# Performance work log

Hardware: AMD Instinct MI355X
Metric: run time of the kernel (lower is better)

The kernel has to match this reference:

```python
import jax, jax.numpy as jnp
import numpy as np

B, N_IN, N_OUT, K, V = 8, 2048, 2048, 64, 64


def setup_inputs() -> dict:
    key = jax.random.key(0)
    k1, k2, k3 = jax.random.split(key, 3)
    return {
        "key": jax.random.normal(k1, (B, N_IN, 1, K), dtype=jnp.float32),
        "query": jax.random.normal(k2, (B, 1, N_OUT, K), dtype=jnp.float32),
        "value": jax.random.normal(k3, (B, N_IN, V), dtype=jnp.float32),
    }


def reference(key, query, value):
    ks = key.shape[-1]
    # sum(key * query, 3) / sqrt(key_size)  ==  batched GEMM over key_size
    # weights: [B, n_inputs, n_outputs]
    weights = jnp.einsum("bik,bok->bio", key[:, :, 0, :], query[:, 0, :, :]) / jnp.sqrt(
        jnp.asarray(ks, dtype=key.dtype)
    )
    weights = jax.nn.softmax(weights, axis=1)  # softmax over n_inputs
    # sum(weights[...,None] * value[:,:,None,:], 1) -> [B, n_outputs, value_size]
    vals = jnp.einsum("bio,biv->bov", weights, value)
    # row-wise L2 normalize each [value_size] vector
    vals = vals / (jnp.linalg.norm(vals, axis=-1, keepdims=True) + 1e-12)
    values = jnp.swapaxes(vals, 1, 2)  # [B, value_size, n_outputs]
    return values, weights
```

## Files before the change

### kernel.cpp

```cpp
#include <hip/hip_runtime.h>

#define NB 8
#define NN 2048
#define KK 64
#define VV 64
#define TO 64
#define IT 64
#define NSTEP (NN / IT)
#define SCALE 0.18033688011112043f

typedef __bf16 bfrag __attribute__((ext_vector_type(8)));
typedef float f32x4 __attribute__((ext_vector_type(4)));
typedef unsigned short u16x4 __attribute__((ext_vector_type(4)));
typedef unsigned short u16x8 __attribute__((ext_vector_type(8)));

__device__ __forceinline__ unsigned short bf16r(float f) {
  unsigned u = __float_as_uint(f);
  u += 0x7fffu + ((u >> 16) & 1u);
  return (unsigned short)(u >> 16);
}

__device__ __forceinline__ int swz(int row, int colByte) {
  return row * 128 + (colByte ^ ((row & 7) << 4));
}

__device__ __forceinline__ bfrag lds_frag(const unsigned short* base, int row, int colByte) {
  return *reinterpret_cast<const bfrag*>(reinterpret_cast<const char*>(base) + swz(row, colByte));
}

struct KS { float4 f[4]; };
__device__ __forceinline__ void k_load(KS& s, const float* __restrict__ g) {
  const float4* p = reinterpret_cast<const float4*>(g);
  s.f[0] = p[0]; s.f[1] = p[1]; s.f[2] = p[2]; s.f[3] = p[3];
}
__device__ __forceinline__ void k_write(const KS& s, unsigned short* lds, int row, int colByte) {
  const float* f = reinterpret_cast<const float*>(&s.f[0]);
  u16x8 a, b;
#pragma unroll
  for (int j = 0; j < 8; ++j) a[j] = bf16r(f[j]);
#pragma unroll
  for (int j = 0; j < 8; ++j) b[j] = bf16r(f[8 + j]);
  *reinterpret_cast<u16x8*>(reinterpret_cast<char*>(lds) + swz(row, colByte)) = a;
  *reinterpret_cast<u16x8*>(reinterpret_cast<char*>(lds) + swz(row, colByte + 16)) = b;
}

struct VS { float4 f[4]; };
__device__ __forceinline__ void v_load(VS& s, const float* __restrict__ g) {
  const float4* p = reinterpret_cast<const float4*>(g);
  s.f[0] = p[0]; s.f[1] = p[1];
  const float4* q = reinterpret_cast<const float4*>(g + VV);
  s.f[2] = q[0]; s.f[3] = q[1];
}
__device__ __forceinline__ void v_write(const VS& s, unsigned short* lds, int il, int v0) {
  const float* lo = reinterpret_cast<const float*>(&s.f[0]);
  const float* hi = reinterpret_cast<const float*>(&s.f[2]);
#pragma unroll
  for (int j = 0; j < 8; ++j) {
    unsigned pk = (unsigned)bf16r(lo[j]) | ((unsigned)bf16r(hi[j]) << 16);
    *reinterpret_cast<unsigned*>(reinterpret_cast<char*>(lds) + swz(v0 + j, il * 2)) = pk;
  }
}

__global__ void __launch_bounds__(256) attn_fused(
    const float* __restrict__ key, const float* __restrict__ query,
    const float* __restrict__ value, float* __restrict__ out)
{
  __shared__ __align__(16) unsigned short Kt[2][IT * KK];
  __shared__ __align__(16) unsigned short Vt[2][VV * IT];
  __shared__ __align__(16) unsigned short Qt[TO * KK];
  __shared__ __align__(16) unsigned short Et[TO * IT];
  __shared__ float Red[4][TO];
  __shared__ float BcD[TO];
  __shared__ float BcN[TO];

  const int tid  = threadIdx.x;
  const int lane = tid & 63;
  const int wv   = tid >> 6;
  const int l15  = lane & 15;
  const int l4   = lane >> 4;

  const int b  = blockIdx.x & 7;
  const int o0 = (blockIdx.x >> 3) * TO;

  const float* Kg = key   + (size_t)b * NN * KK;
  const float* Qg = query + (size_t)b * NN * KK;
  const float* Vg = value + (size_t)b * NN * VV;
  float* outV = out + (size_t)b * VV * NN;
  float* outW = out + (size_t)NB * VV * NN + (size_t)b * NN * NN;

  const int krow = tid >> 2;
  const int kel  = (tid & 3) * 16;
  const int kcb  = (tid & 3) * 32;
  const int vil  = (tid & 31) * 2;
  const int vv0  = (tid >> 5) * 8;

  {
    KS qs;
    k_load(qs, Qg + (size_t)(o0 + krow) * KK + kel);
    k_write(qs, Qt, krow, kcb);
  }
  KS ks; VS vs;
  k_load(ks, Kg + (size_t)krow * KK + kel);
  v_load(vs, Vg + (size_t)vil * VV + vv0);
  k_write(ks, Kt[0], krow, kcb);
  v_write(vs, Vt[0], vil, vv0);
  __syncthreads();

  f32x4 uacc[4];
  float Dacc[4] = {0.f, 0.f, 0.f, 0.f};
#pragma unroll
  for (int s = 0; s < 4; ++s) { f32x4 z = {0.f, 0.f, 0.f, 0.f}; uacc[s] = z; }

  for (int t = 0; t < NSTEP; ++t) {
    const int c = t & 1;
    if (t + 1 < NSTEP) {
      k_load(ks, Kg + (size_t)((t + 1) * IT + krow) * KK + kel);
      v_load(vs, Vg + (size_t)((t + 1) * IT + vil) * VV + vv0);
    }
    bfrag a0 = lds_frag(Kt[c], wv * 16 + l15, l4 * 16);
    bfrag a1 = lds_frag(Kt[c], wv * 16 + l15, 64 + l4 * 16);
#pragma unroll
    for (int s = 0; s < 4; ++s) {
      bfrag b0 = lds_frag(Qt, s * 16 + l15, l4 * 16);
      bfrag b1 = lds_frag(Qt, s * 16 + l15, 64 + l4 * 16);
      f32x4 z = {0.f, 0.f, 0.f, 0.f};
      z = __builtin_amdgcn_mfma_f32_16x16x32_bf16(a0, b0, z, 0, 0, 0);
      z = __builtin_amdgcn_mfma_f32_16x16x32_bf16(a1, b1, z, 0, 0, 0);
      f32x4 e;
#pragma unroll
      for (int r = 0; r < 4; ++r) e[r] = exp2f(z[r] * SCALE);
      Dacc[s] += e[0] + e[1] + e[2] + e[3];
      u16x4 pk;
#pragma unroll
      for (int r = 0; r < 4; ++r) pk[r] = bf16r(e[r]);
      *reinterpret_cast<u16x4*>(reinterpret_cast<char*>(Et) +
                                swz(s * 16 + l15, wv * 32 + l4 * 8)) = pk;
    }
    if (t + 1 < NSTEP) {
      k_write(ks, Kt[c ^ 1], krow, kcb);
      v_write(vs, Vt[c ^ 1], vil, vv0);
    }
    __syncthreads();
    bfrag va0 = lds_frag(Vt[c], wv * 16 + l15, l4 * 16);
    bfrag va1 = lds_frag(Vt[c], wv * 16 + l15, 64 + l4 * 16);
#pragma unroll
    for (int s = 0; s < 4; ++s) {
      bfrag e0 = lds_frag(Et, s * 16 + l15, l4 * 16);
      bfrag e1 = lds_frag(Et, s * 16 + l15, 64 + l4 * 16);
      uacc[s] = __builtin_amdgcn_mfma_f32_16x16x32_bf16(va0, e0, uacc[s], 0, 0, 0);
      uacc[s] = __builtin_amdgcn_mfma_f32_16x16x32_bf16(va1, e1, uacc[s], 0, 0, 0);
    }
    __syncthreads();
  }

#pragma unroll
  for (int s = 0; s < 4; ++s) {
    float d = Dacc[s];
    d += __shfl_xor(d, 16, 64);
    d += __shfl_xor(d, 32, 64);
    if (lane < 16) Red[wv][s * 16 + lane] = d;
  }
  __syncthreads();
  if (tid < TO) {
    float D = Red[0][tid] + Red[1][tid] + Red[2][tid] + Red[3][tid];
    BcD[tid] = 1.0f / D;
  }
  __syncthreads();
  float invd[4];
#pragma unroll
  for (int s = 0; s < 4; ++s) invd[s] = BcD[s * 16 + l15];
  __syncthreads();

#pragma unroll
  for (int s = 0; s < 4; ++s) {
    float ss = uacc[s][0] * uacc[s][0] + uacc[s][1] * uacc[s][1] +
               uacc[s][2] * uacc[s][2] + uacc[s][3] * uacc[s][3];
    ss += __shfl_xor(ss, 16, 64);
    ss += __shfl_xor(ss, 32, 64);
    if (lane < 16) Red[wv][s * 16 + lane] = ss;
  }
  __syncthreads();
  if (tid < TO) {
    float n = Red[0][tid] + Red[1][tid] + Red[2][tid] + Red[3][tid];
    BcN[tid] = 1.0f / (sqrtf(n) + 1e-12f);
  }
  __syncthreads();
#pragma unroll
  for (int s = 0; s < 4; ++s) {
    float inn = BcN[s * 16 + l15];
    float* vp = outV + (size_t)(wv * 16 + l4 * 4) * NN + o0 + s * 16 + l15;
#pragma unroll
    for (int r = 0; r < 4; ++r) vp[(size_t)r * NN] = uacc[s][r] * inn;
  }

  k_load(ks, Kg + (size_t)krow * KK + kel);
  k_write(ks, Kt[0], krow, kcb);
  __syncthreads();
  for (int t = 0; t < NSTEP; ++t) {
    const int c = t & 1;
    if (t + 1 < NSTEP)
      k_load(ks, Kg + (size_t)((t + 1) * IT + krow) * KK + kel);
    bfrag a0 = lds_frag(Kt[c], wv * 16 + l15, l4 * 16);
    bfrag a1 = lds_frag(Kt[c], wv * 16 + l15, 64 + l4 * 16);
#pragma unroll
    for (int s = 0; s < 4; ++s) {
      bfrag b0 = lds_frag(Qt, s * 16 + l15, l4 * 16);
      bfrag b1 = lds_frag(Qt, s * 16 + l15, 64 + l4 * 16);
      f32x4 z = {0.f, 0.f, 0.f, 0.f};
      z = __builtin_amdgcn_mfma_f32_16x16x32_bf16(a0, b0, z, 0, 0, 0);
      z = __builtin_amdgcn_mfma_f32_16x16x32_bf16(a1, b1, z, 0, 0, 0);
      float* wp = outW + (size_t)(t * IT + wv * 16 + l4 * 4) * NN + o0 + s * 16 + l15;
#pragma unroll
      for (int r = 0; r < 4; ++r)
        wp[(size_t)r * NN] = exp2f(z[r] * SCALE) * invd[s];
    }
    if (t + 1 < NSTEP) k_write(ks, Kt[c ^ 1], krow, kcb);
    __syncthreads();
  }
}

extern "C" void kernel_launch(void* const* d_in, const int* in_sizes, int n_in,
                              void* d_out, int out_size, void* d_ws, size_t ws_size,
                              hipStream_t stream) {
  (void)in_sizes; (void)n_in; (void)d_ws; (void)ws_size; (void)out_size;
  const float* key   = (const float*)d_in[0];
  const float* query = (const float*)d_in[1];
  const float* value = (const float*)d_in[2];
  float* out = (float*)d_out;
  attn_fused<<<dim3(NB * (NN / TO)), dim3(256), 0, stream>>>(key, query, value, out);
}
```

Before: 84.53 us.

## Split fused attention into split-input pass, reduction, and tiled weights kernels

The single fused kernel (256 blocks, each serially sweeping all 2048 inputs twice) is replaced by three kernels. The first splits the input dimension into 4 chunks (1024 blocks) that write partial value accumulators and softmax denominators into scratch held inside the weights output region. A small reduce kernel then combines the partials, normalizes, and writes the values and inverse denominators to the workspace. A separate 128x128-tiled kernel recomputes the logits and writes normalized weights. The aim is more parallelism and better occupancy. The cost is two extra launches, scratch traffic through global memory, and single-buffered LDS in pass 1.

```diff
diff --git a/kernel.cpp b/kernel.cpp
--- a/kernel.cpp
+++ b/kernel.cpp
@@ -4,9 +4,6 @@
 #define NN 2048
 #define KK 64
 #define VV 64
-#define TO 64
-#define IT 64
-#define NSTEP (NN / IT)
 #define SCALE 0.18033688011112043f
 
 typedef __bf16 bfrag __attribute__((ext_vector_type(8)));
@@ -61,17 +58,20 @@
   }
 }
 
-__global__ void __launch_bounds__(256) attn_fused(
+#define CHUNK 512
+#define IT 64
+#define K1STEPS (CHUNK / IT)
+#define SCR_STRIDE 4160
+
+__global__ void __launch_bounds__(256) attn_pass1(
     const float* __restrict__ key, const float* __restrict__ query,
-    const float* __restrict__ value, float* __restrict__ out)
+    const float* __restrict__ value, float* __restrict__ scratch)
 {
-  __shared__ __align__(16) unsigned short Kt[2][IT * KK];
-  __shared__ __align__(16) unsigned short Vt[2][VV * IT];
-  __shared__ __align__(16) unsigned short Qt[TO * KK];
-  __shared__ __align__(16) unsigned short Et[TO * IT];
-  __shared__ float Red[4][TO];
-  __shared__ float BcD[TO];
-  __shared__ float BcN[TO];
+  __shared__ __align__(16) unsigned short Kt[IT * KK];
+  __shared__ __align__(16) unsigned short Vt[VV * IT];
+  __shared__ __align__(16) unsigned short Qt[64 * KK];
+  __shared__ __align__(16) unsigned short Et[64 * IT];
+  __shared__ float Red[4][64];
 
   const int tid  = threadIdx.x;
   const int lane = tid & 63;
@@ -79,14 +79,17 @@
   const int l15  = lane & 15;
   const int l4   = lane >> 4;
 
-  const int b  = blockIdx.x & 7;
-  const int o0 = (blockIdx.x >> 3) * TO;
+  const int b    = blockIdx.x & 7;
+  const int rest = blockIdx.x >> 3;
+  const int ot   = rest & 31;
+  const int ci   = rest >> 5;
+  const int o0   = ot * 64;
+  const int ib0  = ci * CHUNK;
 
   const float* Kg = key   + (size_t)b * NN * KK;
   const float* Qg = query + (size_t)b * NN * KK;
   const float* Vg = value + (size_t)b * NN * VV;
-  float* outV = out + (size_t)b * VV * NN;
-  float* outW = out + (size_t)NB * VV * NN + (size_t)b * NN * NN;
+  float* scr = scratch + (size_t)((b * 32 + ot) * 4 + ci) * SCR_STRIDE;
 
   const int krow = tid >> 2;
   const int kel  = (tid & 3) * 16;
@@ -100,10 +103,10 @@
     k_write(qs, Qt, krow, kcb);
   }
   KS ks; VS vs;
-  k_load(ks, Kg + (size_t)krow * KK + kel);
-  v_load(vs, Vg + (size_t)vil * VV + vv0);
-  k_write(ks, Kt[0], krow, kcb);
-  v_write(vs, Vt[0], vil, vv0);
+  k_load(ks, Kg + (size_t)(ib0 + krow) * KK + kel);
+  v_load(vs, Vg + (size_t)(ib0 + vil) * VV + vv0);
+  k_write(ks, Kt, krow, kcb);
+  v_write(vs, Vt, vil, vv0);
   __syncthreads();
 
   f32x4 uacc[4];
@@ -111,14 +114,13 @@
 #pragma unroll
   for (int s = 0; s < 4; ++s) { f32x4 z = {0.f, 0.f, 0.f, 0.f}; uacc[s] = z; }
 
-  for (int t = 0; t < NSTEP; ++t) {
-    const int c = t & 1;
-    if (t + 1 < NSTEP) {
-      k_load(ks, Kg + (size_t)((t + 1) * IT + krow) * KK + kel);
-      v_load(vs, Vg + (size_t)((t + 1) * IT + vil) * VV + vv0);
-    }
-    bfrag a0 = lds_frag(Kt[c], wv * 16 + l15, l4 * 16);
-    bfrag a1 = lds_frag(Kt[c], wv * 16 + l15, 64 + l4 * 16);
+  for (int t = 0; t < K1STEPS; ++t) {
+    if (t + 1 < K1STEPS) {
+      k_load(ks, Kg + (size_t)(ib0 + (t + 1) * IT + krow) * KK + kel);
+      v_load(vs, Vg + (size_t)(ib0 + (t + 1) * IT + vil) * VV + vv0);
+    }
+    bfrag a0 = lds_frag(Kt, wv * 16 + l15, l4 * 16);
+    bfrag a1 = lds_frag(Kt, wv * 16 + l15, 64 + l4 * 16);
 #pragma unroll
     for (int s = 0; s < 4; ++s) {
       bfrag b0 = lds_frag(Qt, s * 16 + l15, l4 * 16);
@@ -136,13 +138,10 @@
       *reinterpret_cast<u16x4*>(reinterpret_cast<char*>(Et) +
                                 swz(s * 16 + l15, wv * 32 + l4 * 8)) = pk;
     }
-    if (t + 1 < NSTEP) {
-      k_write(ks, Kt[c ^ 1], krow, kcb);
-      v_write(vs, Vt[c ^ 1], vil, vv0);
-    }
     __syncthreads();
-    bfrag va0 = lds_frag(Vt[c], wv * 16 + l15, l4 * 16);
-    bfrag va1 = lds_frag(Vt[c], wv * 16 + l15, 64 + l4 * 16);
+    if (t + 1 < K1STEPS) k_write(ks, Kt, krow, kcb);
+    bfrag va0 = lds_frag(Vt, wv * 16 + l15, l4 * 16);
+    bfrag va1 = lds_frag(Vt, wv * 16 + l15, 64 + l4 * 16);
 #pragma unroll
     for (int s = 0; s < 4; ++s) {
       bfrag e0 = lds_frag(Et, s * 16 + l15, l4 * 16);
@@ -151,7 +150,14 @@
       uacc[s] = __builtin_amdgcn_mfma_f32_16x16x32_bf16(va1, e1, uacc[s], 0, 0, 0);
     }
     __syncthreads();
-  }
+    if (t + 1 < K1STEPS) v_write(vs, Vt, vil, vv0);
+  }
+
+#pragma unroll
+  for (int s = 0; s < 4; ++s)
+#pragma unroll
+    for (int r = 0; r < 4; ++r)
+      scr[(wv * 16 + l4 * 4 + r) * 64 + s * 16 + l15] = uacc[s][r];
 
 #pragma unroll
   for (int s = 0; s < 4; ++s) {
@@ -161,71 +167,146 @@
     if (lane < 16) Red[wv][s * 16 + lane] = d;
   }
   __syncthreads();
-  if (tid < TO) {
-    float D = Red[0][tid] + Red[1][tid] + Red[2][tid] + Red[3][tid];
-    BcD[tid] = 1.0f / D;
-  }
-  __syncthreads();
-  float invd[4];
-#pragma unroll
-  for (int s = 0; s < 4; ++s) invd[s] = BcD[s * 16 + l15];
-  __syncthreads();
-
-#pragma unroll
-  for (int s = 0; s < 4; ++s) {
-    float ss = uacc[s][0] * uacc[s][0] + uacc[s][1] * uacc[s][1] +
-               uacc[s][2] * uacc[s][2] + uacc[s][3] * uacc[s][3];
-    ss += __shfl_xor(ss, 16, 64);
-    ss += __shfl_xor(ss, 32, 64);
-    if (lane < 16) Red[wv][s * 16 + lane] = ss;
-  }
-  __syncthreads();
-  if (tid < TO) {
-    float n = Red[0][tid] + Red[1][tid] + Red[2][tid] + Red[3][tid];
-    BcN[tid] = 1.0f / (sqrtf(n) + 1e-12f);
-  }
-  __syncthreads();
-#pragma unroll
-  for (int s = 0; s < 4; ++s) {
-    float inn = BcN[s * 16 + l15];
-    float* vp = outV + (size_t)(wv * 16 + l4 * 4) * NN + o0 + s * 16 + l15;
-#pragma unroll
-    for (int r = 0; r < 4; ++r) vp[(size_t)r * NN] = uacc[s][r] * inn;
-  }
-
-  k_load(ks, Kg + (size_t)krow * KK + kel);
-  k_write(ks, Kt[0], krow, kcb);
-  __syncthreads();
-  for (int t = 0; t < NSTEP; ++t) {
-    const int c = t & 1;
-    if (t + 1 < NSTEP)
-      k_load(ks, Kg + (size_t)((t + 1) * IT + krow) * KK + kel);
-    bfrag a0 = lds_frag(Kt[c], wv * 16 + l15, l4 * 16);
-    bfrag a1 = lds_frag(Kt[c], wv * 16 + l15, 64 + l4 * 16);
-#pragma unroll
-    for (int s = 0; s < 4; ++s) {
-      bfrag b0 = lds_frag(Qt, s * 16 + l15, l4 * 16);
-      bfrag b1 = lds_frag(Qt, s * 16 + l15, 64 + l4 * 16);
-      f32x4 z = {0.f, 0.f, 0.f, 0.f};
-      z = __builtin_amdgcn_mfma_f32_16x16x32_bf16(a0, b0, z, 0, 0, 0);
-      z = __builtin_amdgcn_mfma_f32_16x16x32_bf16(a1, b1, z, 0, 0, 0);
-      float* wp = outW + (size_t)(t * IT + wv * 16 + l4 * 4) * NN + o0 + s * 16 + l15;
+  if (tid < 64)
+    scr[4096 + tid] = Red[0][tid] + Red[1][tid] + Red[2][tid] + Red[3][tid];
+}
+
+__global__ void __launch_bounds__(256) attn_reduce(
+    const float* __restrict__ scratch, float* __restrict__ outV,
+    float* __restrict__ invD)
+{
+  __shared__ float R2[4][64];
+  __shared__ float Nn[64];
+
+  const int tid = threadIdx.x;
+  const int b   = blockIdx.x & 7;
+  const int ot  = blockIdx.x >> 3;
+  const float* base = scratch + (size_t)(b * 32 + ot) * 4 * SCR_STRIDE;
+
+  const int ol = tid & 63;
+  const int vb = tid >> 6;
+
+  float u[16];
+#pragma unroll
+  for (int j = 0; j < 16; ++j) u[j] = 0.f;
+#pragma unroll
+  for (int c = 0; c < 4; ++c) {
+    const float* p = base + c * SCR_STRIDE;
+#pragma unroll
+    for (int j = 0; j < 16; ++j) u[j] += p[tid + j * 256];
+  }
+  float ssq = 0.f;
+#pragma unroll
+  for (int j = 0; j < 16; ++j) ssq += u[j] * u[j];
+  R2[vb][ol] = ssq;
+  __syncthreads();
+  if (tid < 64) {
+    float n = R2[0][tid] + R2[1][tid] + R2[2][tid] + R2[3][tid];
+    Nn[tid] = 1.f / (sqrtf(n) + 1e-12f);
+    float D = 0.f;
+#pragma unroll
+    for (int c = 0; c < 4; ++c) D += base[c * SCR_STRIDE + 4096 + tid];
+    invD[b * NN + ot * 64 + tid] = 1.f / D;
+  }
+  __syncthreads();
+  const float inn = Nn[ol];
+  float* vp = outV + (size_t)b * VV * NN + ot * 64 + ol;
+#pragma unroll
+  for (int j = 0; j < 16; ++j)
+    vp[(size_t)(vb + 4 * j) * NN] = u[j] * inn;
+}
+
+__global__ void __launch_bounds__(256) attn_weights(
+    const float* __restrict__ key, const float* __restrict__ query,
+    const float* __restrict__ invD, float* __restrict__ outWall)
+{
+  __shared__ __align__(16) unsigned short Kt2[128 * 64];
+  __shared__ __align__(16) unsigned short Qt2[128 * 64];
+
+  const int tid  = threadIdx.x;
+  const int lane = tid & 63;
+  const int wv   = tid >> 6;
+  const int l15  = lane & 15;
+  const int l4   = lane >> 4;
+
+  const int b    = blockIdx.x & 7;
+  const int rest = blockIdx.x >> 3;
+  const int it   = rest & 15;
+  const int ot   = rest >> 4;
+
+  const float* Kg = key   + (size_t)b * NN * KK;
+  const float* Qg = query + (size_t)b * NN * KK;
+  float* outW = outWall + (size_t)b * NN * NN;
+
+  const int krow = tid >> 2;
+  const int kel  = (tid & 3) * 16;
+  const int kcb  = (tid & 3) * 32;
+
+  KS s0, s1, s2, s3;
+  k_load(s0, Kg + (size_t)(it * 128 + krow) * KK + kel);
+  k_load(s1, Kg + (size_t)(it * 128 + 64 + krow) * KK + kel);
+  k_load(s2, Qg + (size_t)(ot * 128 + krow) * KK + kel);
+  k_load(s3, Qg + (size_t)(ot * 128 + 64 + krow) * KK + kel);
+  k_write(s0, Kt2, krow, kcb);
+  k_write(s1, Kt2, krow + 64, kcb);
+  k_write(s2, Qt2, krow, kcb);
+  k_write(s3, Qt2, krow + 64, kcb);
+
+  float invd[8];
+#pragma unroll
+  for (int s = 0; s < 8; ++s)
+    invd[s] = invD[b * NN + ot * 128 + s * 16 + l15];
+  __syncthreads();
+
+  bfrag a0[2], a1[2];
+#pragma unroll
+  for (int m = 0; m < 2; ++m) {
+    a0[m] = lds_frag(Kt2, wv * 32 + m * 16 + l15, l4 * 16);
+    a1[m] = lds_frag(Kt2, wv * 32 + m * 16 + l15, 64 + l4 * 16);
+  }
+  f32x4 acc[2][8];
+#pragma unroll
+  for (int m = 0; m < 2; ++m)
+#pragma unroll
+    for (int s = 0; s < 8; ++s) { f32x4 z = {0.f, 0.f, 0.f, 0.f}; acc[m][s] = z; }
+
+#pragma unroll
+  for (int s = 0; s < 8; ++s) {
+    bfrag b0 = lds_frag(Qt2, s * 16 + l15, l4 * 16);
+    bfrag b1 = lds_frag(Qt2, s * 16 + l15, 64 + l4 * 16);
+#pragma unroll
+    for (int m = 0; m < 2; ++m) {
+      acc[m][s] = __builtin_amdgcn_mfma_f32_16x16x32_bf16(a0[m], b0, acc[m][s], 0, 0, 0);
+      acc[m][s] = __builtin_amdgcn_mfma_f32_16x16x32_bf16(a1[m], b1, acc[m][s], 0, 0, 0);
+    }
+  }
+
+#pragma unroll
+  for (int m = 0; m < 2; ++m)
+#pragma unroll
+    for (int s = 0; s < 8; ++s) {
+      float* wp = outW + (size_t)(it * 128 + wv * 32 + m * 16 + l4 * 4) * NN +
+                  ot * 128 + s * 16 + l15;
 #pragma unroll
       for (int r = 0; r < 4; ++r)
-        wp[(size_t)r * NN] = exp2f(z[r] * SCALE) * invd[s];
-    }
-    if (t + 1 < NSTEP) k_write(ks, Kt[c ^ 1], krow, kcb);
-    __syncthreads();
-  }
+        wp[(size_t)r * NN] = exp2f(acc[m][s][r] * SCALE) * invd[s];
+    }
 }
 
 extern "C" void kernel_launch(void* const* d_in, const int* in_sizes, int n_in,
                               void* d_out, int out_size, void* d_ws, size_t ws_size,
                               hipStream_t stream) {
-  (void)in_sizes; (void)n_in; (void)d_ws; (void)ws_size; (void)out_size;
+  (void)in_sizes; (void)n_in; (void)ws_size; (void)out_size;
   const float* key   = (const float*)d_in[0];
   const float* query = (const float*)d_in[1];
   const float* value = (const float*)d_in[2];
-  float* out = (float*)d_out;
-  attn_fused<<<dim3(NB * (NN / TO)), dim3(256), 0, stream>>>(key, query, value, out);
-}
+  float* out  = (float*)d_out;
+  float* outV = out;
+  float* outW = out + (size_t)NB * VV * NN;
+  float* invD = (float*)d_ws;
+  float* scratch = outW;
+
+  attn_pass1 <<<dim3(NB * 32 * 4), dim3(256), 0, stream>>>(key, query, value, scratch);
+  attn_reduce<<<dim3(NB * 32),     dim3(256), 0, stream>>>(scratch, outV, invD);
+  attn_weights<<<dim3(NB * 16 * 16), dim3(256), 0, stream>>>(key, query, invD, outW);
+}
```

After: 70.97 us. 16.0% less time.

## Restructure fused attention into 32-output tiles with 512-thread blocks and register softmax

Applied to the files above, without the earlier changes.

Output tiles shrink from 64 to 32 columns and blocks grow to 512 threads, doubling the grid. Query fragments now stay in registers instead of shared memory. The exp tile is laid out so the exponentiated scores feed the value MFMA straight from registers, which removes the intermediate Et shared buffer and one barrier per step. The weights are written as float4 along the output dimension rather than scalar strided stores, and bf16 conversion uses native casts. The costs are a split-i reduction through shared memory at the end and recomputing K·Q on a smaller tile, which means more redundant K loads per output.

```diff
diff --git a/kernel.cpp b/kernel.cpp
--- a/kernel.cpp
+++ b/kernel.cpp
@@ -4,21 +4,13 @@
 #define NN 2048
 #define KK 64
 #define VV 64
-#define TO 64
-#define IT 64
-#define NSTEP (NN / IT)
+#define OS 32
+#define NT 32
 #define SCALE 0.18033688011112043f
+#define USTRIDE 36
 
 typedef __bf16 bfrag __attribute__((ext_vector_type(8)));
-typedef float f32x4 __attribute__((ext_vector_type(4)));
-typedef unsigned short u16x4 __attribute__((ext_vector_type(4)));
-typedef unsigned short u16x8 __attribute__((ext_vector_type(8)));
-
-__device__ __forceinline__ unsigned short bf16r(float f) {
-  unsigned u = __float_as_uint(f);
-  u += 0x7fffu + ((u >> 16) & 1u);
-  return (unsigned short)(u >> 16);
-}
+typedef float  f32x4 __attribute__((ext_vector_type(4)));
 
 __device__ __forceinline__ int swz(int row, int colByte) {
   return row * 128 + (colByte ^ ((row & 7) << 4));
@@ -26,6 +18,15 @@
 
 __device__ __forceinline__ bfrag lds_frag(const unsigned short* base, int row, int colByte) {
   return *reinterpret_cast<const bfrag*>(reinterpret_cast<const char*>(base) + swz(row, colByte));
+}
+
+__device__ __forceinline__ bfrag g_frag(const float* __restrict__ g) {
+  const float4* p = reinterpret_cast<const float4*>(g);
+  float4 x = p[0], y = p[1];
+  bfrag r;
+  r[0] = (__bf16)x.x; r[1] = (__bf16)x.y; r[2] = (__bf16)x.z; r[3] = (__bf16)x.w;
+  r[4] = (__bf16)y.x; r[5] = (__bf16)y.y; r[6] = (__bf16)y.z; r[7] = (__bf16)y.w;
+  return r;
 }
 
 struct KS { float4 f[4]; };
@@ -35,13 +36,13 @@
 }
 __device__ __forceinline__ void k_write(const KS& s, unsigned short* lds, int row, int colByte) {
   const float* f = reinterpret_cast<const float*>(&s.f[0]);
-  u16x8 a, b;
-#pragma unroll
-  for (int j = 0; j < 8; ++j) a[j] = bf16r(f[j]);
-#pragma unroll
-  for (int j = 0; j < 8; ++j) b[j] = bf16r(f[8 + j]);
-  *reinterpret_cast<u16x8*>(reinterpret_cast<char*>(lds) + swz(row, colByte)) = a;
-  *reinterpret_cast<u16x8*>(reinterpret_cast<char*>(lds) + swz(row, colByte + 16)) = b;
+  bfrag a, b;
+#pragma unroll
+  for (int j = 0; j < 8; ++j) a[j] = (__bf16)f[j];
+#pragma unroll
+  for (int j = 0; j < 8; ++j) b[j] = (__bf16)f[8 + j];
+  *reinterpret_cast<bfrag*>(reinterpret_cast<char*>(lds) + swz(row, colByte)) = a;
+  *reinterpret_cast<bfrag*>(reinterpret_cast<char*>(lds) + swz(row, colByte + 16)) = b;
 }
 
 struct VS { float4 f[4]; };
@@ -56,31 +57,38 @@
   const float* hi = reinterpret_cast<const float*>(&s.f[2]);
 #pragma unroll
   for (int j = 0; j < 8; ++j) {
-    unsigned pk = (unsigned)bf16r(lo[j]) | ((unsigned)bf16r(hi[j]) << 16);
-    *reinterpret_cast<unsigned*>(reinterpret_cast<char*>(lds) + swz(v0 + j, il * 2)) = pk;
-  }
-}
-
-__global__ void __launch_bounds__(256) attn_fused(
+    __bf16 two[2] = { (__bf16)lo[j], (__bf16)hi[j] };
+    *reinterpret_cast<unsigned*>(reinterpret_cast<char*>(lds) + swz(v0 + j, il * 2)) =
+        *reinterpret_cast<unsigned*>(two);
+  }
+}
+
+__global__ void __launch_bounds__(512, 4) attn_fused(
     const float* __restrict__ key, const float* __restrict__ query,
     const float* __restrict__ value, float* __restrict__ out)
 {
-  __shared__ __align__(16) unsigned short Kt[2][IT * KK];
-  __shared__ __align__(16) unsigned short Vt[2][VV * IT];
-  __shared__ __align__(16) unsigned short Qt[TO * KK];
-  __shared__ __align__(16) unsigned short Et[TO * IT];
-  __shared__ float Red[4][TO];
-  __shared__ float BcD[TO];
-  __shared__ float BcN[TO];
+  __shared__ __align__(16) char smem[32768];
+  __shared__ float Red[4][16];
+  __shared__ float InvD[OS];
+  __shared__ float Nn[OS];
+  unsigned short* Kt0 = reinterpret_cast<unsigned short*>(smem);
+  unsigned short* Kt1 = reinterpret_cast<unsigned short*>(smem + 8192);
+  unsigned short* Vt0 = reinterpret_cast<unsigned short*>(smem + 16384);
+  unsigned short* Vt1 = reinterpret_cast<unsigned short*>(smem + 24576);
+  float* U0 = reinterpret_cast<float*>(smem);
+  float* U1 = reinterpret_cast<float*>(smem + 9216);
 
   const int tid  = threadIdx.x;
   const int lane = tid & 63;
-  const int wv   = tid >> 6;
+  const int w    = tid >> 6;
   const int l15  = lane & 15;
   const int l4   = lane >> 4;
+  const int vhalf = w & 1;
+  const int ihalf = (w >> 1) & 1;
+  const int oh    = w >> 2;
 
   const int b  = blockIdx.x & 7;
-  const int o0 = (blockIdx.x >> 3) * TO;
+  const int o0 = (blockIdx.x >> 3) * OS;
 
   const float* Kg = key   + (size_t)b * NN * KK;
   const float* Qg = query + (size_t)b * NN * KK;
@@ -88,133 +96,157 @@
   float* outV = out + (size_t)b * VV * NN;
   float* outW = out + (size_t)NB * VV * NN + (size_t)b * NN * NN;
 
+  bfrag qb0, qb1;
+  {
+    const float* qr = Qg + (size_t)(o0 + oh * 16 + l15) * KK;
+    qb0 = g_frag(qr + l4 * 8);
+    qb1 = g_frag(qr + 32 + l4 * 8);
+  }
+
   const int krow = tid >> 2;
   const int kel  = (tid & 3) * 16;
   const int kcb  = (tid & 3) * 32;
-  const int vil  = (tid & 31) * 2;
-  const int vv0  = (tid >> 5) * 8;
-
-  {
-    KS qs;
-    k_load(qs, Qg + (size_t)(o0 + krow) * KK + kel);
-    k_write(qs, Qt, krow, kcb);
-  }
+  const int t2   = tid & 255;
+  const int vil  = (t2 & 31) * 2;
+  const int vv0  = (t2 >> 5) * 8;
+
   KS ks; VS vs;
-  k_load(ks, Kg + (size_t)krow * KK + kel);
-  v_load(vs, Vg + (size_t)vil * VV + vv0);
-  k_write(ks, Kt[0], krow, kcb);
-  v_write(vs, Vt[0], vil, vv0);
-  __syncthreads();
-
-  f32x4 uacc[4];
-  float Dacc[4] = {0.f, 0.f, 0.f, 0.f};
-#pragma unroll
-  for (int s = 0; s < 4; ++s) { f32x4 z = {0.f, 0.f, 0.f, 0.f}; uacc[s] = z; }
-
-  for (int t = 0; t < NSTEP; ++t) {
-    const int c = t & 1;
-    if (t + 1 < NSTEP) {
-      k_load(ks, Kg + (size_t)((t + 1) * IT + krow) * KK + kel);
-      v_load(vs, Vg + (size_t)((t + 1) * IT + vil) * VV + vv0);
-    }
-    bfrag a0 = lds_frag(Kt[c], wv * 16 + l15, l4 * 16);
-    bfrag a1 = lds_frag(Kt[c], wv * 16 + l15, 64 + l4 * 16);
-#pragma unroll
-    for (int s = 0; s < 4; ++s) {
-      bfrag b0 = lds_frag(Qt, s * 16 + l15, l4 * 16);
-      bfrag b1 = lds_frag(Qt, s * 16 + l15, 64 + l4 * 16);
-      f32x4 z = {0.f, 0.f, 0.f, 0.f};
-      z = __builtin_amdgcn_mfma_f32_16x16x32_bf16(a0, b0, z, 0, 0, 0);
-      z = __builtin_amdgcn_mfma_f32_16x16x32_bf16(a1, b1, z, 0, 0, 0);
-      f32x4 e;
-#pragma unroll
-      for (int r = 0; r < 4; ++r) e[r] = exp2f(z[r] * SCALE);
-      Dacc[s] += e[0] + e[1] + e[2] + e[3];
-      u16x4 pk;
-#pragma unroll
-      for (int r = 0; r < 4; ++r) pk[r] = bf16r(e[r]);
-      *reinterpret_cast<u16x4*>(reinterpret_cast<char*>(Et) +
-                                swz(s * 16 + l15, wv * 32 + l4 * 8)) = pk;
-    }
-    if (t + 1 < NSTEP) {
-      k_write(ks, Kt[c ^ 1], krow, kcb);
-      v_write(vs, Vt[c ^ 1], vil, vv0);
+  if (tid < 256) { k_load(ks, Kg + (size_t)krow * KK + kel); }
+  else           { v_load(vs, Vg + (size_t)vil * VV + vv0); }
+  if (tid < 256) k_write(ks, Kt0, krow, kcb);
+  else           v_write(vs, Vt0, vil, vv0);
+  __syncthreads();
+
+  const int ip = (l15 & 3) + ((l15 >> 2) * 8);
+
+  f32x4 uacc[2];
+  { f32x4 z = {0.f,0.f,0.f,0.f}; uacc[0] = z; uacc[1] = z; }
+  float Dacc = 0.f;
+
+  for (int t = 0; t < NT; ++t) {
+    unsigned short* Kc = (t & 1) ? Kt1 : Kt0;
+    unsigned short* Vc = (t & 1) ? Vt1 : Vt0;
+    unsigned short* Kn = (t & 1) ? Kt0 : Kt1;
+    unsigned short* Vn = (t & 1) ? Vt0 : Vt1;
+    if (t + 1 < NT) {
+      if (tid < 256) k_load(ks, Kg + (size_t)((t + 1) * 64 + krow) * KK + kel);
+      else           v_load(vs, Vg + (size_t)((t + 1) * 64 + vil) * VV + vv0);
+    }
+    const int r1 = ihalf * 32 + ip;
+    bfrag ka10 = lds_frag(Kc, r1,     l4 * 16);
+    bfrag ka11 = lds_frag(Kc, r1,     64 + l4 * 16);
+    bfrag ka20 = lds_frag(Kc, r1 + 4, l4 * 16);
+    bfrag ka21 = lds_frag(Kc, r1 + 4, 64 + l4 * 16);
+    f32x4 z1 = {0.f,0.f,0.f,0.f}, z2 = {0.f,0.f,0.f,0.f};
+    z1 = __builtin_amdgcn_mfma_f32_16x16x32_bf16(ka10, qb0, z1, 0, 0, 0);
+    z1 = __builtin_amdgcn_mfma_f32_16x16x32_bf16(ka11, qb1, z1, 0, 0, 0);
+    z2 = __builtin_amdgcn_mfma_f32_16x16x32_bf16(ka20, qb0, z2, 0, 0, 0);
+    z2 = __builtin_amdgcn_mfma_f32_16x16x32_bf16(ka21, qb1, z2, 0, 0, 0);
+    f32x4 e1, e2;
+#pragma unroll
+    for (int r = 0; r < 4; ++r) e1[r] = exp2f(z1[r] * SCALE);
+#pragma unroll
+    for (int r = 0; r < 4; ++r) e2[r] = exp2f(z2[r] * SCALE);
+    Dacc += e1[0] + e1[1] + e1[2] + e1[3] + e2[0] + e2[1] + e2[2] + e2[3];
+    bfrag eb;
+#pragma unroll
+    for (int r = 0; r < 4; ++r) eb[r]     = (__bf16)e1[r];
+#pragma unroll
+    for (int r = 0; r < 4; ++r) eb[4 + r] = (__bf16)e2[r];
+#pragma unroll
+    for (int vg = 0; vg < 2; ++vg) {
+      bfrag va = lds_frag(Vc, vhalf * 32 + vg * 16 + l15, ihalf * 64 + l4 * 16);
+      uacc[vg] = __builtin_amdgcn_mfma_f32_16x16x32_bf16(va, eb, uacc[vg], 0, 0, 0);
+    }
+    if (t + 1 < NT) {
+      if (tid < 256) k_write(ks, Kn, krow, kcb);
+      else           v_write(vs, Vn, vil, vv0);
     }
     __syncthreads();
-    bfrag va0 = lds_frag(Vt[c], wv * 16 + l15, l4 * 16);
-    bfrag va1 = lds_frag(Vt[c], wv * 16 + l15, 64 + l4 * 16);
-#pragma unroll
-    for (int s = 0; s < 4; ++s) {
-      bfrag e0 = lds_frag(Et, s * 16 + l15, l4 * 16);
-      bfrag e1 = lds_frag(Et, s * 16 + l15, 64 + l4 * 16);
-      uacc[s] = __builtin_amdgcn_mfma_f32_16x16x32_bf16(va0, e0, uacc[s], 0, 0, 0);
-      uacc[s] = __builtin_amdgcn_mfma_f32_16x16x32_bf16(va1, e1, uacc[s], 0, 0, 0);
-    }
-    __syncthreads();
-  }
-
-#pragma unroll
-  for (int s = 0; s < 4; ++s) {
-    float d = Dacc[s];
+  }
+
+  {
+    float d = Dacc;
     d += __shfl_xor(d, 16, 64);
     d += __shfl_xor(d, 32, 64);
-    if (lane < 16) Red[wv][s * 16 + lane] = d;
-  }
-  __syncthreads();
-  if (tid < TO) {
-    float D = Red[0][tid] + Red[1][tid] + Red[2][tid] + Red[3][tid];
-    BcD[tid] = 1.0f / D;
-  }
-  __syncthreads();
-  float invd[4];
-#pragma unroll
-  for (int s = 0; s < 4; ++s) invd[s] = BcD[s * 16 + l15];
-  __syncthreads();
-
-#pragma unroll
-  for (int s = 0; s < 4; ++s) {
-    float ss = uacc[s][0] * uacc[s][0] + uacc[s][1] * uacc[s][1] +
-               uacc[s][2] * uacc[s][2] + uacc[s][3] * uacc[s][3];
-    ss += __shfl_xor(ss, 16, 64);
-    ss += __shfl_xor(ss, 32, 64);
-    if (lane < 16) Red[wv][s * 16 + lane] = ss;
-  }
-  __syncthreads();
-  if (tid < TO) {
-    float n = Red[0][tid] + Red[1][tid] + Red[2][tid] + Red[3][tid];
-    BcN[tid] = 1.0f / (sqrtf(n) + 1e-12f);
-  }
-  __syncthreads();
-#pragma unroll
-  for (int s = 0; s < 4; ++s) {
-    float inn = BcN[s * 16 + l15];
-    float* vp = outV + (size_t)(wv * 16 + l4 * 4) * NN + o0 + s * 16 + l15;
-#pragma unroll
-    for (int r = 0; r < 4; ++r) vp[(size_t)r * NN] = uacc[s][r] * inn;
-  }
-
-  k_load(ks, Kg + (size_t)krow * KK + kel);
-  k_write(ks, Kt[0], krow, kcb);
-  __syncthreads();
-  for (int t = 0; t < NSTEP; ++t) {
-    const int c = t & 1;
-    if (t + 1 < NSTEP)
-      k_load(ks, Kg + (size_t)((t + 1) * IT + krow) * KK + kel);
-    bfrag a0 = lds_frag(Kt[c], wv * 16 + l15, l4 * 16);
-    bfrag a1 = lds_frag(Kt[c], wv * 16 + l15, 64 + l4 * 16);
-#pragma unroll
-    for (int s = 0; s < 4; ++s) {
-      bfrag b0 = lds_frag(Qt, s * 16 + l15, l4 * 16);
-      bfrag b1 = lds_frag(Qt, s * 16 + l15, 64 + l4 * 16);
-      f32x4 z = {0.f, 0.f, 0.f, 0.f};
-      z = __builtin_amdgcn_mfma_f32_16x16x32_bf16(a0, b0, z, 0, 0, 0);
-      z = __builtin_amdgcn_mfma_f32_16x16x32_bf16(a1, b1, z, 0, 0, 0);
-      float* wp = outW + (size_t)(t * IT + wv * 16 + l4 * 4) * NN + o0 + s * 16 + l15;
+    if ((w & 1) == 0 && lane < 16) Red[w >> 1][lane] = d;
+  }
+  {
+    float* Ur = ihalf ? U1 : U0;
+#pragma unroll
+    for (int vg = 0; vg < 2; ++vg)
 #pragma unroll
       for (int r = 0; r < 4; ++r)
-        wp[(size_t)r * NN] = exp2f(z[r] * SCALE) * invd[s];
-    }
-    if (t + 1 < NSTEP) k_write(ks, Kt[c ^ 1], krow, kcb);
+        Ur[(vhalf * 32 + vg * 16 + l4 * 4 + r) * USTRIDE + oh * 16 + l15] = uacc[vg][r];
+  }
+  __syncthreads();
+  {
+    const int v = tid >> 3, o = (tid & 7) * 4;
+    f32x4 a = *reinterpret_cast<f32x4*>(&U0[v * USTRIDE + o]);
+    f32x4 c = *reinterpret_cast<f32x4*>(&U1[v * USTRIDE + o]);
+    a = a + c;
+    *reinterpret_cast<f32x4*>(&U0[v * USTRIDE + o]) = a;
+  }
+  __syncthreads();
+  if (tid < OS) {
+    float ssq = 0.f;
+#pragma unroll
+    for (int v = 0; v < VV; ++v) { float x = U0[v * USTRIDE + tid]; ssq += x * x; }
+    Nn[tid] = 1.f / (sqrtf(ssq) + 1e-12f);
+  } else if (tid < 2 * OS) {
+    const int o = tid - OS, ohh = o >> 4;
+    InvD[o] = 1.f / (Red[ohh * 2][o & 15] + Red[ohh * 2 + 1][o & 15]);
+  }
+  __syncthreads();
+  {
+    const int v = tid >> 3, o = (tid & 7) * 4;
+    f32x4 a  = *reinterpret_cast<f32x4*>(&U0[v * USTRIDE + o]);
+    f32x4 nn = *reinterpret_cast<f32x4*>(&Nn[o]);
+    f32x4 r;
+#pragma unroll
+    for (int j = 0; j < 4; ++j) r[j] = a[j] * nn[j];
+    *reinterpret_cast<f32x4*>(&outV[(size_t)v * NN + o0 + o]) = r;
+  }
+  f32x4 id = *reinterpret_cast<f32x4*>(&InvD[oh * 16 + l4 * 4]);
+  __syncthreads();
+
+  const int iq    = w & 3;
+  const int kbrow = tid >> 3;
+  const int kseg  = tid & 7;
+  {
+    const float4* kp = reinterpret_cast<const float4*>(Kg + (size_t)kbrow * KK + kseg * 8);
+    float4 p0 = kp[0], p1 = kp[1];
+    bfrag f;
+    f[0] = (__bf16)p0.x; f[1] = (__bf16)p0.y; f[2] = (__bf16)p0.z; f[3] = (__bf16)p0.w;
+    f[4] = (__bf16)p1.x; f[5] = (__bf16)p1.y; f[6] = (__bf16)p1.z; f[7] = (__bf16)p1.w;
+    *reinterpret_cast<bfrag*>(reinterpret_cast<char*>(Kt0) + swz(kbrow, kseg * 16)) = f;
+  }
+  __syncthreads();
+  for (int t = 0; t < NT; ++t) {
+    unsigned short* Kc = (t & 1) ? Kt1 : Kt0;
+    unsigned short* Kn = (t & 1) ? Kt0 : Kt1;
+    float4 p0, p1;
+    if (t + 1 < NT) {
+      const float4* kp = reinterpret_cast<const float4*>(
+          Kg + (size_t)((t + 1) * 64 + kbrow) * KK + kseg * 8);
+      p0 = kp[0]; p1 = kp[1];
+    }
+    bfrag kb0 = lds_frag(Kc, iq * 16 + l15, l4 * 16);
+    bfrag kb1 = lds_frag(Kc, iq * 16 + l15, 64 + l4 * 16);
+    f32x4 z = {0.f,0.f,0.f,0.f};
+    z = __builtin_amdgcn_mfma_f32_16x16x32_bf16(qb0, kb0, z, 0, 0, 0);
+    z = __builtin_amdgcn_mfma_f32_16x16x32_bf16(qb1, kb1, z, 0, 0, 0);
+    f32x4 ww;
+#pragma unroll
+    for (int r = 0; r < 4; ++r) ww[r] = exp2f(z[r] * SCALE) * id[r];
+    float* wp = outW + (size_t)(t * 64 + iq * 16 + l15) * NN + o0 + oh * 16 + l4 * 4;
+    *reinterpret_cast<f32x4*>(wp) = ww;
+    if (t + 1 < NT) {
+      bfrag f;
+      f[0] = (__bf16)p0.x; f[1] = (__bf16)p0.y; f[2] = (__bf16)p0.z; f[3] = (__bf16)p0.w;
+      f[4] = (__bf16)p1.x; f[5] = (__bf16)p1.y; f[6] = (__bf16)p1.z; f[7] = (__bf16)p1.w;
+      *reinterpret_cast<bfrag*>(reinterpret_cast<char*>(Kn) + swz(kbrow, kseg * 16)) = f;
+    }
     __syncthreads();
   }
 }
@@ -227,5 +259,5 @@
   const float* query = (const float*)d_in[1];
   const float* value = (const float*)d_in[2];
   float* out = (float*)d_out;
-  attn_fused<<<dim3(NB * (NN / TO)), dim3(256), 0, stream>>>(key, query, value, out);
-}
+  attn_fused<<<dim3(NB * (NN / OS)), dim3(512), 0, stream>>>(key, query, value, out);
+}
```

Result: faster. 78.70 us (-6.9%).
